# Kernel optimization log

Hardware: AMD Instinct MI355X
Metric: run time of the kernel (lower is better)

Reference implementation:

```python
import jax, jax.numpy as jnp
import numpy as np

CH_IN = 256
CA = CH_IN // 8   # attention channels (theta/phi)
CH = CH_IN // 2   # value channels (g)


def _maxpool2(t):
    # 2x2 max pool, stride 2: (B,C,H,W) -> (B,C,H//2,W//2)
    b, c, h, w = t.shape
    return t.reshape(b, c, h // 2, 2, w // 2, 2).max(axis=(3, 5))


def setup_inputs() -> dict:
    key = jax.random.key(0)
    ks = jax.random.split(key, 6)
    B, H, W = 16, 64, 64
    x = jax.random.normal(ks[0], (B, CH_IN, H, W), dtype=jnp.float32)
    # 1x1 conv weights stored as (out_ch, in_ch); spectral_norm is a weight
    # reparameterization, so the forward math is a plain conv with these weights.
    s = 0.05
    w_theta = jax.random.normal(ks[1], (CA, CH_IN), dtype=jnp.float32) * s
    w_phi = jax.random.normal(ks[2], (CA, CH_IN), dtype=jnp.float32) * s
    w_g = jax.random.normal(ks[3], (CH, CH_IN), dtype=jnp.float32) * s
    w_o = jax.random.normal(ks[4], (CH_IN, CH), dtype=jnp.float32) * s
    # gamma is initialized to 0 in the module; use a nonzero value so the
    # attention branch contributes to the output.
    gamma = jnp.asarray(0.5, dtype=jnp.float32)
    return {"x": x, "w_theta": w_theta, "w_phi": w_phi, "w_g": w_g,
            "w_o": w_o, "gamma": gamma}


def reference(x, w_theta, w_phi, w_g, w_o, gamma):
    B, C, H, W = x.shape
    # 1x1 convs as channel contractions
    theta = jnp.einsum('oc,bchw->bohw', w_theta, x)            # (B,CA,H,W)
    phi = _maxpool2(jnp.einsum('oc,bchw->bohw', w_phi, x))     # (B,CA,H/2,W/2)
    g = _maxpool2(jnp.einsum('oc,bchw->bohw', w_g, x))         # (B,CH,H/2,W/2)
    N = H * W
    M = N // 4
    theta = theta.reshape(B, CA, N)
    phi = phi.reshape(B, CA, M)
    g = g.reshape(B, CH, M)
    # beta = softmax(theta^T phi) over keys (no scaling, as in original)
    beta = jax.nn.softmax(jnp.einsum('bcn,bcm->bnm', theta, phi), axis=-1)  # (B,N,M)
    o = jnp.einsum('bcm,bnm->bcn', g, beta).reshape(B, CH, H, W)
    o = jnp.einsum('oc,bchw->bohw', w_o, o)                    # (B,C,H,W)
    return gamma * o + x
```

## Files before the change

### kernel.cpp

```cpp
#include <hip/hip_runtime.h>
#include <hip/hip_bf16.h>

#define NB 16
#define CIN 256
#define CA 32
#define CH 128
#define NN 4096
#define MM 1024

typedef __attribute__((ext_vector_type(8))) short s16x8;
typedef __attribute__((ext_vector_type(4))) float f32x4;

static __device__ __forceinline__ unsigned short f2bf(float x) {
  __hip_bfloat16 h = __float2bfloat16(x);
  return __builtin_bit_cast(unsigned short, h);
}
static __device__ __forceinline__ float bf2f(unsigned short u) {
  unsigned int v = ((unsigned int)u) << 16;
  return __builtin_bit_cast(float, v);
}
static __device__ __forceinline__ unsigned int pk2(float a, float b) {
  return (unsigned)f2bf(a) | ((unsigned)f2bf(b) << 16);
}
static __device__ __forceinline__ void gload_lds16(const void* g, void* s) {
  __builtin_amdgcn_global_load_lds(
      (const __attribute__((address_space(1))) unsigned int*)g,
      (__attribute__((address_space(3))) unsigned int*)s, 16, 0, 0);
}

__global__ __launch_bounds__(256) void k_wcvt(const float* __restrict__ w_theta,
                                              const float* __restrict__ w_phi,
                                              const float* __restrict__ w_g,
                                              const float* __restrict__ w_o,
                                              unsigned short* __restrict__ wcat2,
                                              unsigned short* __restrict__ wo2) {
  const int i = blockIdx.x * 256 + threadIdx.x;
  if (i < 49152) {
    const int row = i >> 8, c = i & 255;
    const float v = (row < 32) ? w_theta[i]
                  : (row < 64) ? w_phi[i - 8192]
                               : w_g[i - 16384];
    const int dst = ((row >> 4) * 8 + (c >> 5)) * 512 +
                    (((c >> 3) & 3) * 16 + (row & 15)) * 8 + (c & 7);
    wcat2[dst] = f2bf(v);
  } else {
    const int w = i - 49152;
    const int c_out = w >> 7, k = w & 127;
    const int dst = (((c_out >> 4) * 16) + ((k >> 5) * 4) + ((k >> 3) & 3)) * 128 +
                    ((c_out & 15) << 3) + (k & 7);
    wo2[dst] = f2bf(w_o[w]);
  }
}

__global__ __launch_bounds__(512) void k_proj(const float* __restrict__ x,
                                              const unsigned short* __restrict__ wcat2,
                                              unsigned short* __restrict__ theta,
                                              unsigned short* __restrict__ phi2,
                                              unsigned short* __restrict__ g2) {
  __shared__ unsigned short lds[192 * 136];
  unsigned short (*xl)[32][132] = reinterpret_cast<unsigned short(*)[32][132]>(lds);
  unsigned short (*ol)[136] = reinterpret_cast<unsigned short(*)[136]>(lds);
  const int b = blockIdx.y;
  const int t = blockIdx.x;
  const int tid = threadIdx.x;
  const int wv = tid >> 6;
  const int l = tid & 63;
  const int grp = l >> 4, col = l & 15;
  const float* xb = x + (size_t)b * CIN * NN;
  auto STAGEX = [&](int buf, int kc) {
#pragma unroll
    for (int s = 0; s < 2; ++s) {
      const int i = tid + s * 512;
      const int cl = i >> 5, nq = i & 31;
      const float4 v = *reinterpret_cast<const float4*>(
          xb + (size_t)(kc * 32 + cl) * NN + t * 128 + nq * 4);
      *reinterpret_cast<uint2*>(&xl[buf][cl][nq * 4]) =
          make_uint2(pk2(v.x, v.y), pk2(v.z, v.w));
    }
  };
  f32x4 acc[12];
#pragma unroll
  for (int r = 0; r < 12; ++r) acc[r] = f32x4{0.f, 0.f, 0.f, 0.f};
  STAGEX(0, 0);
#pragma unroll 1
  for (int kc = 0; kc < 8; ++kc) {
    __syncthreads();
    if (kc < 7) STAGEX((kc + 1) & 1, kc + 1);
    const int cur = kc & 1;
    s16x8 bfrag;
#pragma unroll
    for (int j = 0; j < 8; ++j)
      bfrag[j] = (short)xl[cur][grp * 8 + j][wv * 16 + col];
#pragma unroll
    for (int r = 0; r < 12; ++r) {
      const s16x8 af = *reinterpret_cast<const s16x8*>(
          wcat2 + (size_t)(r * 8 + kc) * 512 + l * 8);
      acc[r] = __builtin_amdgcn_mfma_f32_16x16x32_bf16(af, bfrag, acc[r], 0, 0, 0);
    }
  }
  __syncthreads();
#pragma unroll
  for (int r = 0; r < 12; ++r)
#pragma unroll
    for (int q = 0; q < 4; ++q)
      ol[r * 16 + grp * 4 + q][wv * 16 + col] = f2bf(acc[r][q]);
  __syncthreads();
  unsigned short* thb = theta + (size_t)b * NN * CA;
  for (int i = tid; i < 128 * 16; i += 512) {
    const int n = i >> 4, cp = (i & 15) << 1;
    const unsigned int v = (unsigned)ol[cp][n] | ((unsigned)ol[cp + 1][n] << 16);
    *reinterpret_cast<unsigned int*>(thb + (size_t)(t * 128 + n) * CA + cp) = v;
  }
  unsigned short* phb2 = phi2 + (size_t)b * MM * CA;
  for (int i = tid; i < 32 * 32; i += 512) {
    const int ca = i & 31, mx = i >> 5;
    const float v = fmaxf(
        fmaxf(bf2f(ol[32 + ca][2 * mx]), bf2f(ol[32 + ca][2 * mx + 1])),
        fmaxf(bf2f(ol[32 + ca][64 + 2 * mx]), bf2f(ol[32 + ca][64 + 2 * mx + 1])));
    const int m = t * 32 + mx;
    phb2[(m >> 4) * 512 + (ca >> 3) * 128 + (m & 15) * 8 + (ca & 7)] = f2bf(v);
  }
  unsigned short* gb2 = g2 + (size_t)b * CH * MM;
  for (int i = tid; i < 128 * 32; i += 512) {
    const int mx = i & 31, c = i >> 5;
    const float v = fmaxf(
        fmaxf(bf2f(ol[64 + c][2 * mx]), bf2f(ol[64 + c][2 * mx + 1])),
        fmaxf(bf2f(ol[64 + c][64 + 2 * mx]), bf2f(ol[64 + c][64 + 2 * mx + 1])));
    const int pg = (mx & 15) >> 2;
    const int pj = (mx & 3) | ((mx >> 4) << 2);
    gb2[(size_t)(t * 8 + (c >> 4)) * 512 + pg * 128 + (c & 15) * 8 + pj] = f2bf(v);
  }
}

__global__ __launch_bounds__(256, 3) void k_attn_out(
    const unsigned short* __restrict__ theta, const unsigned short* __restrict__ phi2,
    const unsigned short* __restrict__ g2, const unsigned short* __restrict__ wo2,
    const float* __restrict__ x, const float* __restrict__ gammap,
    float* __restrict__ out) {
  __shared__ __align__(16) unsigned short kv[2][10240];
  const int b = blockIdx.y;
  const int tid = threadIdx.x;
  const int wv = tid >> 6;
  const int l = tid & 63;
  const int grp = l >> 4, col = l & 15;
  const int n0 = blockIdx.x * 128 + wv * 32;
  const unsigned short* thb = theta + (size_t)b * NN * CA;
  const unsigned short* ph2b = phi2 + (size_t)b * MM * CA;
  const unsigned short* gb2 = g2 + (size_t)b * CH * MM;
  const s16x8 qf0 = *reinterpret_cast<const s16x8*>(thb + (size_t)(n0 + col) * CA + grp * 8);
  const s16x8 qf1 = *reinterpret_cast<const s16x8*>(thb + (size_t)(n0 + 16 + col) * CA + grp * 8);

  auto STAGE = [&](int buf, int tile) {
    const int mc = tile * 64;
    const unsigned short* ksrc = ph2b + (mc >> 4) * 512;
    const unsigned short* vsrc = gb2 + (size_t)(mc >> 5) * 4096;
#pragma unroll
    for (int q = 0; q < 5; ++q) {
      const int i = wv * 5 + q;
      const unsigned short* src = (i < 4) ? (ksrc + i * 512) : (vsrc + (size_t)(i - 4) * 512);
      gload_lds16(src + (size_t)l * 8, &kv[buf][i * 512]);
    }
  };

  f32x4 oa0[8], oa1[8];
#pragma unroll
  for (int t = 0; t < 8; ++t) {
    oa0[t] = f32x4{0.f, 0.f, 0.f, 0.f};
    oa1[t] = f32x4{0.f, 0.f, 0.f, 0.f};
  }
  float m0 = -INFINITY, l0 = 0.f, m1 = -INFINITY, l1 = 0.f;
  const f32x4 z4 = {0.f, 0.f, 0.f, 0.f};

  STAGE(0, 0);
  __syncthreads();
#pragma unroll 1
  for (int it = 0; it < 16; ++it) {
    const int cur = it & 1;
    if (it < 15) STAGE(cur ^ 1, it + 1);
    const unsigned short* kb = &kv[cur][0];
    const unsigned short* vb = &kv[cur][2048];
    const int fo = grp * 128 + col * 8;
    const s16x8 kf0 = *reinterpret_cast<const s16x8*>(kb + 0 * 512 + fo);
    const s16x8 kf1 = *reinterpret_cast<const s16x8*>(kb + 1 * 512 + fo);
    const s16x8 kf2 = *reinterpret_cast<const s16x8*>(kb + 2 * 512 + fo);
    const s16x8 kf3 = *reinterpret_cast<const s16x8*>(kb + 3 * 512 + fo);
    f32x4 s00 = __builtin_amdgcn_mfma_f32_16x16x32_bf16(kf0, qf0, z4, 0, 0, 0);
    f32x4 s01 = __builtin_amdgcn_mfma_f32_16x16x32_bf16(kf1, qf0, z4, 0, 0, 0);
    f32x4 s02 = __builtin_amdgcn_mfma_f32_16x16x32_bf16(kf2, qf0, z4, 0, 0, 0);
    f32x4 s03 = __builtin_amdgcn_mfma_f32_16x16x32_bf16(kf3, qf0, z4, 0, 0, 0);
    f32x4 s10 = __builtin_amdgcn_mfma_f32_16x16x32_bf16(kf0, qf1, z4, 0, 0, 0);
    f32x4 s11 = __builtin_amdgcn_mfma_f32_16x16x32_bf16(kf1, qf1, z4, 0, 0, 0);
    f32x4 s12 = __builtin_amdgcn_mfma_f32_16x16x32_bf16(kf2, qf1, z4, 0, 0, 0);
    f32x4 s13 = __builtin_amdgcn_mfma_f32_16x16x32_bf16(kf3, qf1, z4, 0, 0, 0);
    float cm0 = -INFINITY, cm1 = -INFINITY;
#pragma unroll
    for (int r = 0; r < 4; ++r) {
      cm0 = fmaxf(cm0, fmaxf(fmaxf(s00[r], s01[r]), fmaxf(s02[r], s03[r])));
      cm1 = fmaxf(cm1, fmaxf(fmaxf(s10[r], s11[r]), fmaxf(s12[r], s13[r])));
    }
    cm0 = fmaxf(cm0, __shfl_xor(cm0, 16));
    cm0 = fmaxf(cm0, __shfl_xor(cm0, 32));
    cm1 = fmaxf(cm1, __shfl_xor(cm1, 16));
    cm1 = fmaxf(cm1, __shfl_xor(cm1, 32));
    if (!__all(cm0 <= m0 + 8.f && cm1 <= m1 + 8.f)) {
      const float mn0 = fmaxf(m0, cm0), mn1 = fmaxf(m1, cm1);
      const float sc0 = __expf(m0 - mn0), sc1 = __expf(m1 - mn1);
      l0 *= sc0;
      l1 *= sc1;
#pragma unroll
      for (int t = 0; t < 8; ++t) {
#pragma unroll
        for (int r = 0; r < 4; ++r) {
          oa0[t][r] *= sc0;
          oa1[t][r] *= sc1;
        }
      }
      m0 = mn0;
      m1 = mn1;
    }
    s16x8 pfA0, pfB0, pfA1, pfB1;
    {
      float p0[4], p1[4], p2[4], p3[4];
      float cs = 0.f;
#pragma unroll
      for (int r = 0; r < 4; ++r) {
        p0[r] = __expf(s00[r] - m0);
        p1[r] = __expf(s01[r] - m0);
        p2[r] = __expf(s02[r] - m0);
        p3[r] = __expf(s03[r] - m0);
        cs += (p0[r] + p1[r]) + (p2[r] + p3[r]);
      }
      cs += __shfl_xor(cs, 16);
      cs += __shfl_xor(cs, 32);
      l0 += cs;
      const uint4 ua = make_uint4(pk2(p0[0], p0[1]), pk2(p0[2], p0[3]),
                                  pk2(p1[0], p1[1]), pk2(p1[2], p1[3]));
      const uint4 ub = make_uint4(pk2(p2[0], p2[1]), pk2(p2[2], p2[3]),
                                  pk2(p3[0], p3[1]), pk2(p3[2], p3[3]));
      pfA0 = __builtin_bit_cast(s16x8, ua);
      pfB0 = __builtin_bit_cast(s16x8, ub);
    }
    {
      float p0[4], p1[4], p2[4], p3[4];
      float cs = 0.f;
#pragma unroll
      for (int r = 0; r < 4; ++r) {
        p0[r] = __expf(s10[r] - m1);
        p1[r] = __expf(s11[r] - m1);
        p2[r] = __expf(s12[r] - m1);
        p3[r] = __expf(s13[r] - m1);
        cs += (p0[r] + p1[r]) + (p2[r] + p3[r]);
      }
      cs += __shfl_xor(cs, 16);
      cs += __shfl_xor(cs, 32);
      l1 += cs;
      const uint4 ua = make_uint4(pk2(p0[0], p0[1]), pk2(p0[2], p0[3]),
                                  pk2(p1[0], p1[1]), pk2(p1[2], p1[3]));
      const uint4 ub = make_uint4(pk2(p2[0], p2[1]), pk2(p2[2], p2[3]),
                                  pk2(p3[0], p3[1]), pk2(p3[2], p3[3]));
      pfA1 = __builtin_bit_cast(s16x8, ua);
      pfB1 = __builtin_bit_cast(s16x8, ub);
    }
#pragma unroll
    for (int t = 0; t < 8; ++t) {
      const s16x8 vfA = *reinterpret_cast<const s16x8*>(vb + t * 512 + fo);
      const s16x8 vfB = *reinterpret_cast<const s16x8*>(vb + 4096 + t * 512 + fo);
      oa0[t] = __builtin_amdgcn_mfma_f32_16x16x32_bf16(vfA, pfA0, oa0[t], 0, 0, 0);
      oa0[t] = __builtin_amdgcn_mfma_f32_16x16x32_bf16(vfB, pfB0, oa0[t], 0, 0, 0);
      oa1[t] = __builtin_amdgcn_mfma_f32_16x16x32_bf16(vfA, pfA1, oa1[t], 0, 0, 0);
      oa1[t] = __builtin_amdgcn_mfma_f32_16x16x32_bf16(vfB, pfB1, oa1[t], 0, 0, 0);
    }
    __syncthreads();
  }
  unsigned short* obw = &kv[0][0] + (size_t)wv * (32 * 136);
  const float ri0 = 1.f / l0, ri1 = 1.f / l1;
#pragma unroll
  for (int t = 0; t < 8; ++t) {
    *reinterpret_cast<uint2*>(obw + col * 136 + t * 16 + grp * 4) =
        make_uint2(pk2(oa0[t][0] * ri0, oa0[t][1] * ri0),
                   pk2(oa0[t][2] * ri0, oa0[t][3] * ri0));
    *reinterpret_cast<uint2*>(obw + (16 + col) * 136 + t * 16 + grp * 4) =
        make_uint2(pk2(oa1[t][0] * ri1, oa1[t][1] * ri1),
                   pk2(oa1[t][2] * ri1, oa1[t][3] * ri1));
  }
  s16x8 of0[4], of1[4];
#pragma unroll
  for (int ks = 0; ks < 4; ++ks) {
    of0[ks] = *reinterpret_cast<const s16x8*>(obw + col * 136 + ks * 32 + grp * 8);
    of1[ks] = *reinterpret_cast<const s16x8*>(obw + (16 + col) * 136 + ks * 32 + grp * 8);
  }
  const float gamma = gammap[0];
  const float* xb2 = x + (size_t)b * CIN * NN;
  float* outb = out + (size_t)b * CIN * NN;
#pragma unroll 1
  for (int t2 = 0; t2 < 16; ++t2) {
    f32x4 a20 = {0.f, 0.f, 0.f, 0.f};
    f32x4 a21 = {0.f, 0.f, 0.f, 0.f};
#pragma unroll
    for (int ks = 0; ks < 4; ++ks) {
      const s16x8 wf = *reinterpret_cast<const s16x8*>(
          wo2 + (size_t)(t2 * 16 + ks * 4 + grp) * 128 + col * 8);
      a20 = __builtin_amdgcn_mfma_f32_16x16x32_bf16(wf, of0[ks], a20, 0, 0, 0);
      a21 = __builtin_amdgcn_mfma_f32_16x16x32_bf16(wf, of1[ks], a21, 0, 0, 0);
    }
#pragma unroll
    for (int r = 0; r < 4; ++r) {
      const size_t idx = (size_t)(t2 * 16 + grp * 4 + r) * NN + n0 + col;
      outb[idx] = fmaf(gamma, a20[r], xb2[idx]);
      outb[idx + 16] = fmaf(gamma, a21[r], xb2[idx + 16]);
    }
  }
}

extern "C" void kernel_launch(void* const* d_in, const int* in_sizes, int n_in,
                              void* d_out, int out_size, void* d_ws, size_t ws_size,
                              hipStream_t stream) {
  const float* x = (const float*)d_in[0];
  const float* w_theta = (const float*)d_in[1];
  const float* w_phi = (const float*)d_in[2];
  const float* w_g = (const float*)d_in[3];
  const float* w_o = (const float*)d_in[4];
  const float* gamma = (const float*)d_in[5];
  float* out = (float*)d_out;
  char* ws = (char*)d_ws;
  unsigned short* theta = (unsigned short*)(ws + 0);
  unsigned short* phi2 = (unsigned short*)(ws + 4194304);
  unsigned short* g2 = (unsigned short*)(ws + 5242880);
  unsigned short* wo2 = (unsigned short*)(ws + 9437184);
  unsigned short* wcat2 = (unsigned short*)(ws + 9502720);

  k_wcvt<<<dim3(320), 256, 0, stream>>>(w_theta, w_phi, w_g, w_o, wcat2, wo2);
  k_proj<<<dim3(NN / 128, NB), 512, 0, stream>>>(x, wcat2, theta, phi2, g2);
  k_attn_out<<<dim3(NN / 128, NB), 256, 0, stream>>>(theta, phi2, g2, wo2, x, gamma, out);
}
```

Before: 81.75 us.

## Split attention block into 8 waves of 16 queries each

The attention+output kernel now launches 512 threads per block, and each wave handles 16 query rows instead of 32. This halves per-wave accumulator registers and doubles wave count for more latency hiding. Staging of the K/V tiles is redistributed across 8 waves. The trade-off is that each K/V fragment read from LDS feeds half as many MFMAs per wave, and the output-projection weights are loaded by twice as many waves.

```diff
diff --git a/kernel.cpp b/kernel.cpp
--- a/kernel.cpp
+++ b/kernel.cpp
@@ -132,7 +132,7 @@
   }
 }
 
-__global__ __launch_bounds__(256, 3) void k_attn_out(
+__global__ __launch_bounds__(512, 4) void k_attn_out(
     const unsigned short* __restrict__ theta, const unsigned short* __restrict__ phi2,
     const unsigned short* __restrict__ g2, const unsigned short* __restrict__ wo2,
     const float* __restrict__ x, const float* __restrict__ gammap,
@@ -143,32 +143,30 @@
   const int wv = tid >> 6;
   const int l = tid & 63;
   const int grp = l >> 4, col = l & 15;
-  const int n0 = blockIdx.x * 128 + wv * 32;
+  const int n0 = blockIdx.x * 128 + wv * 16;
   const unsigned short* thb = theta + (size_t)b * NN * CA;
   const unsigned short* ph2b = phi2 + (size_t)b * MM * CA;
   const unsigned short* gb2 = g2 + (size_t)b * CH * MM;
-  const s16x8 qf0 = *reinterpret_cast<const s16x8*>(thb + (size_t)(n0 + col) * CA + grp * 8);
-  const s16x8 qf1 = *reinterpret_cast<const s16x8*>(thb + (size_t)(n0 + 16 + col) * CA + grp * 8);
+  const s16x8 qf = *reinterpret_cast<const s16x8*>(thb + (size_t)(n0 + col) * CA + grp * 8);
 
   auto STAGE = [&](int buf, int tile) {
     const int mc = tile * 64;
     const unsigned short* ksrc = ph2b + (mc >> 4) * 512;
     const unsigned short* vsrc = gb2 + (size_t)(mc >> 5) * 4096;
 #pragma unroll
-    for (int q = 0; q < 5; ++q) {
-      const int i = wv * 5 + q;
-      const unsigned short* src = (i < 4) ? (ksrc + i * 512) : (vsrc + (size_t)(i - 4) * 512);
-      gload_lds16(src + (size_t)l * 8, &kv[buf][i * 512]);
+    for (int q = 0; q < 3; ++q) {
+      const int i = wv + q * 8;
+      if (i < 20) {
+        const unsigned short* src = (i < 4) ? (ksrc + i * 512) : (vsrc + (size_t)(i - 4) * 512);
+        gload_lds16(src + (size_t)l * 8, &kv[buf][i * 512]);
+      }
     }
   };
 
-  f32x4 oa0[8], oa1[8];
-#pragma unroll
-  for (int t = 0; t < 8; ++t) {
-    oa0[t] = f32x4{0.f, 0.f, 0.f, 0.f};
-    oa1[t] = f32x4{0.f, 0.f, 0.f, 0.f};
-  }
-  float m0 = -INFINITY, l0 = 0.f, m1 = -INFINITY, l1 = 0.f;
+  f32x4 oa[8];
+#pragma unroll
+  for (int t = 0; t < 8; ++t) oa[t] = f32x4{0.f, 0.f, 0.f, 0.f};
+  float m0 = -INFINITY, l0 = 0.f;
   const f32x4 z4 = {0.f, 0.f, 0.f, 0.f};
 
   STAGE(0, 0);
@@ -184,130 +182,83 @@
     const s16x8 kf1 = *reinterpret_cast<const s16x8*>(kb + 1 * 512 + fo);
     const s16x8 kf2 = *reinterpret_cast<const s16x8*>(kb + 2 * 512 + fo);
     const s16x8 kf3 = *reinterpret_cast<const s16x8*>(kb + 3 * 512 + fo);
-    f32x4 s00 = __builtin_amdgcn_mfma_f32_16x16x32_bf16(kf0, qf0, z4, 0, 0, 0);
-    f32x4 s01 = __builtin_amdgcn_mfma_f32_16x16x32_bf16(kf1, qf0, z4, 0, 0, 0);
-    f32x4 s02 = __builtin_amdgcn_mfma_f32_16x16x32_bf16(kf2, qf0, z4, 0, 0, 0);
-    f32x4 s03 = __builtin_amdgcn_mfma_f32_16x16x32_bf16(kf3, qf0, z4, 0, 0, 0);
-    f32x4 s10 = __builtin_amdgcn_mfma_f32_16x16x32_bf16(kf0, qf1, z4, 0, 0, 0);
-    f32x4 s11 = __builtin_amdgcn_mfma_f32_16x16x32_bf16(kf1, qf1, z4, 0, 0, 0);
-    f32x4 s12 = __builtin_amdgcn_mfma_f32_16x16x32_bf16(kf2, qf1, z4, 0, 0, 0);
-    f32x4 s13 = __builtin_amdgcn_mfma_f32_16x16x32_bf16(kf3, qf1, z4, 0, 0, 0);
-    float cm0 = -INFINITY, cm1 = -INFINITY;
+    f32x4 s0 = __builtin_amdgcn_mfma_f32_16x16x32_bf16(kf0, qf, z4, 0, 0, 0);
+    f32x4 s1 = __builtin_amdgcn_mfma_f32_16x16x32_bf16(kf1, qf, z4, 0, 0, 0);
+    f32x4 s2 = __builtin_amdgcn_mfma_f32_16x16x32_bf16(kf2, qf, z4, 0, 0, 0);
+    f32x4 s3 = __builtin_amdgcn_mfma_f32_16x16x32_bf16(kf3, qf, z4, 0, 0, 0);
+    float cm = -INFINITY;
+#pragma unroll
+    for (int r = 0; r < 4; ++r)
+      cm = fmaxf(cm, fmaxf(fmaxf(s0[r], s1[r]), fmaxf(s2[r], s3[r])));
+    cm = fmaxf(cm, __shfl_xor(cm, 16));
+    cm = fmaxf(cm, __shfl_xor(cm, 32));
+    if (!__all(cm <= m0 + 8.f)) {
+      const float mn = fmaxf(m0, cm);
+      const float sc = __expf(m0 - mn);
+      l0 *= sc;
+#pragma unroll
+      for (int t = 0; t < 8; ++t) {
+#pragma unroll
+        for (int r = 0; r < 4; ++r) oa[t][r] *= sc;
+      }
+      m0 = mn;
+    }
+    float p0[4], p1[4], p2[4], p3[4];
+    float cs = 0.f;
 #pragma unroll
     for (int r = 0; r < 4; ++r) {
-      cm0 = fmaxf(cm0, fmaxf(fmaxf(s00[r], s01[r]), fmaxf(s02[r], s03[r])));
-      cm1 = fmaxf(cm1, fmaxf(fmaxf(s10[r], s11[r]), fmaxf(s12[r], s13[r])));
-    }
-    cm0 = fmaxf(cm0, __shfl_xor(cm0, 16));
-    cm0 = fmaxf(cm0, __shfl_xor(cm0, 32));
-    cm1 = fmaxf(cm1, __shfl_xor(cm1, 16));
-    cm1 = fmaxf(cm1, __shfl_xor(cm1, 32));
-    if (!__all(cm0 <= m0 + 8.f && cm1 <= m1 + 8.f)) {
-      const float mn0 = fmaxf(m0, cm0), mn1 = fmaxf(m1, cm1);
-      const float sc0 = __expf(m0 - mn0), sc1 = __expf(m1 - mn1);
-      l0 *= sc0;
-      l1 *= sc1;
-#pragma unroll
-      for (int t = 0; t < 8; ++t) {
-#pragma unroll
-        for (int r = 0; r < 4; ++r) {
-          oa0[t][r] *= sc0;
-          oa1[t][r] *= sc1;
-        }
-      }
-      m0 = mn0;
-      m1 = mn1;
-    }
-    s16x8 pfA0, pfB0, pfA1, pfB1;
-    {
-      float p0[4], p1[4], p2[4], p3[4];
-      float cs = 0.f;
-#pragma unroll
-      for (int r = 0; r < 4; ++r) {
-        p0[r] = __expf(s00[r] - m0);
-        p1[r] = __expf(s01[r] - m0);
-        p2[r] = __expf(s02[r] - m0);
-        p3[r] = __expf(s03[r] - m0);
-        cs += (p0[r] + p1[r]) + (p2[r] + p3[r]);
-      }
-      cs += __shfl_xor(cs, 16);
-      cs += __shfl_xor(cs, 32);
-      l0 += cs;
-      const uint4 ua = make_uint4(pk2(p0[0], p0[1]), pk2(p0[2], p0[3]),
-                                  pk2(p1[0], p1[1]), pk2(p1[2], p1[3]));
-      const uint4 ub = make_uint4(pk2(p2[0], p2[1]), pk2(p2[2], p2[3]),
-                                  pk2(p3[0], p3[1]), pk2(p3[2], p3[3]));
-      pfA0 = __builtin_bit_cast(s16x8, ua);
-      pfB0 = __builtin_bit_cast(s16x8, ub);
-    }
-    {
-      float p0[4], p1[4], p2[4], p3[4];
-      float cs = 0.f;
-#pragma unroll
-      for (int r = 0; r < 4; ++r) {
-        p0[r] = __expf(s10[r] - m1);
-        p1[r] = __expf(s11[r] - m1);
-        p2[r] = __expf(s12[r] - m1);
-        p3[r] = __expf(s13[r] - m1);
-        cs += (p0[r] + p1[r]) + (p2[r] + p3[r]);
-      }
-      cs += __shfl_xor(cs, 16);
-      cs += __shfl_xor(cs, 32);
-      l1 += cs;
-      const uint4 ua = make_uint4(pk2(p0[0], p0[1]), pk2(p0[2], p0[3]),
-                                  pk2(p1[0], p1[1]), pk2(p1[2], p1[3]));
-      const uint4 ub = make_uint4(pk2(p2[0], p2[1]), pk2(p2[2], p2[3]),
-                                  pk2(p3[0], p3[1]), pk2(p3[2], p3[3]));
-      pfA1 = __builtin_bit_cast(s16x8, ua);
-      pfB1 = __builtin_bit_cast(s16x8, ub);
-    }
+      p0[r] = __expf(s0[r] - m0);
+      p1[r] = __expf(s1[r] - m0);
+      p2[r] = __expf(s2[r] - m0);
+      p3[r] = __expf(s3[r] - m0);
+      cs += (p0[r] + p1[r]) + (p2[r] + p3[r]);
+    }
+    cs += __shfl_xor(cs, 16);
+    cs += __shfl_xor(cs, 32);
+    l0 += cs;
+    const uint4 ua = make_uint4(pk2(p0[0], p0[1]), pk2(p0[2], p0[3]),
+                                pk2(p1[0], p1[1]), pk2(p1[2], p1[3]));
+    const uint4 ub = make_uint4(pk2(p2[0], p2[1]), pk2(p2[2], p2[3]),
+                                pk2(p3[0], p3[1]), pk2(p3[2], p3[3]));
+    const s16x8 pfA = __builtin_bit_cast(s16x8, ua);
+    const s16x8 pfB = __builtin_bit_cast(s16x8, ub);
 #pragma unroll
     for (int t = 0; t < 8; ++t) {
       const s16x8 vfA = *reinterpret_cast<const s16x8*>(vb + t * 512 + fo);
       const s16x8 vfB = *reinterpret_cast<const s16x8*>(vb + 4096 + t * 512 + fo);
-      oa0[t] = __builtin_amdgcn_mfma_f32_16x16x32_bf16(vfA, pfA0, oa0[t], 0, 0, 0);
-      oa0[t] = __builtin_amdgcn_mfma_f32_16x16x32_bf16(vfB, pfB0, oa0[t], 0, 0, 0);
-      oa1[t] = __builtin_amdgcn_mfma_f32_16x16x32_bf16(vfA, pfA1, oa1[t], 0, 0, 0);
-      oa1[t] = __builtin_amdgcn_mfma_f32_16x16x32_bf16(vfB, pfB1, oa1[t], 0, 0, 0);
+      oa[t] = __builtin_amdgcn_mfma_f32_16x16x32_bf16(vfA, pfA, oa[t], 0, 0, 0);
+      oa[t] = __builtin_amdgcn_mfma_f32_16x16x32_bf16(vfB, pfB, oa[t], 0, 0, 0);
     }
     __syncthreads();
   }
-  unsigned short* obw = &kv[0][0] + (size_t)wv * (32 * 136);
-  const float ri0 = 1.f / l0, ri1 = 1.f / l1;
+  unsigned short* obw = &kv[0][0] + (size_t)wv * (16 * 136);
+  const float ri = 1.f / l0;
 #pragma unroll
   for (int t = 0; t < 8; ++t) {
     *reinterpret_cast<uint2*>(obw + col * 136 + t * 16 + grp * 4) =
-        make_uint2(pk2(oa0[t][0] * ri0, oa0[t][1] * ri0),
-                   pk2(oa0[t][2] * ri0, oa0[t][3] * ri0));
-    *reinterpret_cast<uint2*>(obw + (16 + col) * 136 + t * 16 + grp * 4) =
-        make_uint2(pk2(oa1[t][0] * ri1, oa1[t][1] * ri1),
-                   pk2(oa1[t][2] * ri1, oa1[t][3] * ri1));
-  }
-  s16x8 of0[4], of1[4];
-#pragma unroll
-  for (int ks = 0; ks < 4; ++ks) {
-    of0[ks] = *reinterpret_cast<const s16x8*>(obw + col * 136 + ks * 32 + grp * 8);
-    of1[ks] = *reinterpret_cast<const s16x8*>(obw + (16 + col) * 136 + ks * 32 + grp * 8);
-  }
+        make_uint2(pk2(oa[t][0] * ri, oa[t][1] * ri),
+                   pk2(oa[t][2] * ri, oa[t][3] * ri));
+  }
+  s16x8 of[4];
+#pragma unroll
+  for (int ks = 0; ks < 4; ++ks)
+    of[ks] = *reinterpret_cast<const s16x8*>(obw + col * 136 + ks * 32 + grp * 8);
   const float gamma = gammap[0];
   const float* xb2 = x + (size_t)b * CIN * NN;
   float* outb = out + (size_t)b * CIN * NN;
 #pragma unroll 1
   for (int t2 = 0; t2 < 16; ++t2) {
-    f32x4 a20 = {0.f, 0.f, 0.f, 0.f};
-    f32x4 a21 = {0.f, 0.f, 0.f, 0.f};
+    f32x4 a2 = {0.f, 0.f, 0.f, 0.f};
 #pragma unroll
     for (int ks = 0; ks < 4; ++ks) {
       const s16x8 wf = *reinterpret_cast<const s16x8*>(
           wo2 + (size_t)(t2 * 16 + ks * 4 + grp) * 128 + col * 8);
-      a20 = __builtin_amdgcn_mfma_f32_16x16x32_bf16(wf, of0[ks], a20, 0, 0, 0);
-      a21 = __builtin_amdgcn_mfma_f32_16x16x32_bf16(wf, of1[ks], a21, 0, 0, 0);
+      a2 = __builtin_amdgcn_mfma_f32_16x16x32_bf16(wf, of[ks], a2, 0, 0, 0);
     }
 #pragma unroll
     for (int r = 0; r < 4; ++r) {
       const size_t idx = (size_t)(t2 * 16 + grp * 4 + r) * NN + n0 + col;
-      outb[idx] = fmaf(gamma, a20[r], xb2[idx]);
-      outb[idx + 16] = fmaf(gamma, a21[r], xb2[idx + 16]);
+      outb[idx] = fmaf(gamma, a2[r], xb2[idx]);
     }
   }
 }
@@ -331,5 +282,5 @@
 
   k_wcvt<<<dim3(320), 256, 0, stream>>>(w_theta, w_phi, w_g, w_o, wcat2, wo2);
   k_proj<<<dim3(NN / 128, NB), 512, 0, stream>>>(x, wcat2, theta, phi2, g2);
-  k_attn_out<<<dim3(NN / 128, NB), 256, 0, stream>>>(theta, phi2, g2, wo2, x, gamma, out);
-}
+  k_attn_out<<<dim3(NN / 128, NB), 512, 0, stream>>>(theta, phi2, g2, wo2, x, gamma, out);
+}
```

New measurement: 78.56 us. -3.9%, faster.
